# Kernel optimization log

Measured on AMD Instinct MI355X. Metric: run time of the kernel, lower is better.

The kernel has to match this reference:

```python
import jax, jax.numpy as jnp
import numpy as np

# ---- static config (mirrors Spectral2xDown.__init__) ----
B, C_IN, C_OUT = 2, 256, 256
H_HI, W_HI = 256, 512
H_LO, W_LO = 128, 256
LMAX = H_LO            # 128
MMAX = W_LO // 2 + 1   # 129
GROUPS = 32
EPS_GN = 1e-5


def _cc_nodes_weights(n):
    """Clenshaw-Curtis nodes x_j=cos(pi*j/(n-1)) and quadrature weights on [-1,1]
    (torch_harmonics 'equiangular' grid)."""
    N = n - 1
    tj = np.pi * np.arange(n) / N
    xj = np.cos(tj)
    ks = np.arange(1, N // 2 + 1)
    b = np.where(2 * ks == N, 1.0, 2.0)
    s = (b / (4.0 * ks**2 - 1.0))[None, :] * np.cos(2.0 * ks[None, :] * tj[:, None])
    w = (2.0 / N) * (1.0 - s.sum(axis=1))
    w[0] = w[-1] = (1.0 / N**2) if (N % 2) else (1.0 / (N**2 - 1.0))
    return xj, w


def _legpoly(mmax, lmax, x):
    """Orthonormal associated Legendre (-1)^m c_lm P_lm(x), shape [mmax,lmax,len(x)]
    (torch_harmonics _precompute_legpoly, norm='ortho', csphase=True)."""
    nmax = max(mmax, lmax)
    vdm = np.zeros((nmax, nmax, len(x)))
    vdm[0, 0] = 1.0 / np.sqrt(4.0 * np.pi)
    for l in range(1, nmax):
        vdm[l - 1, l] = np.sqrt(2 * l + 1) * x * vdm[l - 1, l - 1]
        vdm[l, l] = np.sqrt((2 * l + 1) * (1 + x) * (1 - x) / (2 * l)) * vdm[l - 1, l - 1]
    for l in range(2, nmax):
        for m in range(0, l - 1):
            vdm[m, l] = (x * np.sqrt((2 * l - 1) / (l - m) * (2 * l + 1) / (l + m)) * vdm[m, l - 1]
                         - np.sqrt((l + m - 1) / (l - m) * (2 * l + 1) / (2 * l - 3)
                                   * (l - m - 1) / (l + m)) * vdm[m, l - 2])
    vdm = vdm[:mmax, :lmax].copy()
    for m in range(1, mmax, 2):  # Condon-Shortley phase
        vdm[m] *= -1.0
    return vdm


def _precompute():
    ct_hi, w_hi = _cc_nodes_weights(H_HI)
    pct_hi = _legpoly(MMAX, LMAX, np.flip(np.arccos(ct_hi)) * 0 + np.cos(np.flip(np.arccos(ct_hi))))
    wmat_hi = pct_hi * w_hi[None, None, :]          # quadrature folded in: [M,L,K_hi]
    ct_lo, _ = _cc_nodes_weights(H_LO)
    pct_lo = _legpoly(MMAX, LMAX, np.cos(np.flip(np.arccos(ct_lo))))  # [M,L,K_lo]
    return wmat_hi.astype(np.float32), pct_lo.astype(np.float32)


def setup_inputs() -> dict:
    key = jax.random.key(0)
    k1, k2 = jax.random.split(key, 2)
    x = jax.random.normal(k1, (B, C_IN, H_HI, W_HI), jnp.float32)
    conv_w = jax.random.normal(k2, (C_OUT, C_IN), jnp.float32) / np.sqrt(C_IN)
    conv_b = jnp.zeros((C_OUT,), jnp.float32)
    gamma = jnp.ones((C_OUT,), jnp.float32)
    beta = jnp.zeros((C_OUT,), jnp.float32)
    wmat_hi, pct_lo = _precompute()
    return {"x": x, "conv_w": conv_w, "conv_b": conv_b, "gamma": gamma, "beta": beta,
            "wmat_hi": jnp.asarray(wmat_hi), "pct_lo": jnp.asarray(pct_lo)}


def reference(x, conv_w, conv_b, gamma, beta, wmat_hi, pct_lo):
    # --- forward real SHT on high-res grid (2*pi * rfft(norm='forward') + Legendre quadrature) ---
    X = (2.0 * jnp.pi / W_HI) * jnp.fft.rfft(x, axis=-1)     # [B,C,K_hi,W_HI//2+1]
    X = X[..., :MMAX]                                        # truncate to mmax
    flm_r = jnp.einsum('bckm,mlk->bclm', X.real, wmat_hi)    # [B,C,L,M]
    flm_i = jnp.einsum('bckm,mlk->bclm', X.imag, wmat_hi)
    # --- inverse real SHT on low-res grid ---
    g = (jnp.einsum('bclm,mlk->bckm', flm_r, pct_lo)
         + 1j * jnp.einsum('bclm,mlk->bckm', flm_i, pct_lo))  # [B,C,K_lo,M]
    y = jnp.fft.irfft(g, n=W_LO, axis=-1) * W_LO             # irfft norm='forward'
    # --- 1x1 conv -> GroupNorm(32) -> exact GELU ---
    h = jnp.einsum('bchw,oc->bohw', y, conv_w) + conv_b[None, :, None, None]
    hg = h.reshape(B, GROUPS, C_OUT // GROUPS, H_LO, W_LO)
    mu = hg.mean(axis=(2, 3, 4), keepdims=True)
    var = ((hg - mu) ** 2).mean(axis=(2, 3, 4), keepdims=True)
    hn = ((hg - mu) * jax.lax.rsqrt(var + EPS_GN)).reshape(B, C_OUT, H_LO, W_LO)
    out = hn * gamma[None, :, None, None] + beta[None, :, None, None]
    return jax.nn.gelu(out, approximate=False)
```

## Files before the change

kernel.cpp:

```cpp
#include <hip/hip_runtime.h>
#include <math.h>


#define ROWS_HI 131072
#define ROWS_LO 65536

#define B_FT    0LL
#define B_FIT   262144LL
#define B_WM    393216LL
#define B_PCT   8781824LL
#define B_STATS 12976128LL
#define B_R1    12976640LL
#define B_R2    80085504LL

typedef __attribute__((ext_vector_type(8))) short bf16x8;
typedef __attribute__((ext_vector_type(8))) unsigned short ushort8;
typedef __attribute__((ext_vector_type(4))) unsigned short ushort4v;
typedef __attribute__((ext_vector_type(4))) float f32x4;

__device__ inline unsigned short f2bf(float f){
  unsigned int u = __float_as_uint(f);
  unsigned int r = u + 0x7FFFu + ((u >> 16) & 1u);
  return (unsigned short)(r >> 16);
}
__device__ inline float bf2f(unsigned short h){
  return __uint_as_float(((unsigned int)h) << 16);
}

__global__ __launch_bounds__(256) void k_tables(unsigned char* __restrict__ ws){
  unsigned short* FT  = (unsigned short*)(ws + B_FT);
  unsigned short* FIT = (unsigned short*)(ws + B_FIT);
  float* stats = (float*)(ws + B_STATS);
  int idx = blockIdx.x*256 + threadIdx.x;
  if (idx < 131072){
    int p = idx >> 9, w = idx & 511, m = p >> 1;
    int pr = (m*w) & 511;
    float ang = (float)pr * (float)(2.0*M_PI/512.0);
    float s, c; sincosf(ang, &s, &c);
    const float S = (float)(2.0*M_PI/512.0);
    FT[idx] = f2bf((p & 1) ? (-S*s) : (S*c));
  }
  int i2 = idx - 131072;
  if (i2 >= 0 && i2 < 65536){
    int w = i2 >> 8, p = i2 & 255, m = p >> 1;
    float eps = (m == 0) ? 1.f : 2.f;
    int pr = (m*w) & 255;
    float ang = (float)pr * (float)(2.0*M_PI/256.0);
    float s, c; sincosf(ang, &s, &c);
    FIT[i2] = f2bf((p & 1) ? (-eps*s) : (eps*c));
  }
  int i3 = idx - (131072 + 65536);
  if (i3 >= 0 && i3 < 128) stats[i3] = 0.f;
}

__global__ __launch_bounds__(256) void k_prep(const float* __restrict__ wmat,
                                              const float* __restrict__ pct,
                                              unsigned char* __restrict__ ws){
  unsigned short* WM = (unsigned short*)(ws + B_WM);
  unsigned short* PT = (unsigned short*)(ws + B_PCT);
  int idx = blockIdx.x*256 + threadIdx.x;
  if (idx < 4194304){
    WM[idx] = f2bf(wmat[idx]);
  } else {
    int j = idx - 4194304;
    if (j < 2097152){
      int m = j >> 14, kp = (j >> 7) & 127, l = j & 127;
      PT[j] = f2bf(pct[m*16384 + l*128 + kp]);
    }
  }
}

template<int AMODE, int CMODE, bool BIAS>
__global__ __launch_bounds__(256) void k_gemm(
    const float* __restrict__ Af,
    const unsigned short* __restrict__ Abf,
    const unsigned short* __restrict__ Bt,
    float* __restrict__ Cf,
    unsigned short* __restrict__ Cbf,
    const float* __restrict__ bias,
    int ldA, int ldB, int ldC, int ksteps,
    long long sA, long long sB, int bzsh, long long sC)
{
  __shared__ unsigned short Ah[128][40];
  __shared__ unsigned short Al[128][40];
  __shared__ unsigned short Bs[128][40];
  const int tid = threadIdx.x;
  const int z = blockIdx.z;
  const long long offA = (long long)z * sA;
  const long long offB = (long long)(z >> bzsh) * sB;
  const long long offC = (long long)z * sC;
  const int row0 = blockIdx.x * 128;
  const int n0   = blockIdx.y * 128;
  const int lane = tid & 63;
  const int wv = tid >> 6;
  const int wm = wv >> 1, wn = wv & 1;
  const int fr = lane & 15, q = lane >> 4;
  const int ms = tid >> 1, half = tid & 1;

  f32x4 acc[4][4];
#pragma unroll
  for (int i=0;i<4;++i)
#pragma unroll
    for (int j=0;j<4;++j) acc[i][j] = (f32x4){0.f,0.f,0.f,0.f};

  for (int ks = 0; ks < ksteps; ++ks){
    const int k0 = ks * 32;
    if (AMODE == 0){
      const float* s = Af + offA + (long long)(row0 + ms) * ldA + k0 + half*16;
      float vv[16];
      *(float4*)(vv+0)  = *(const float4*)(s+0);
      *(float4*)(vv+4)  = *(const float4*)(s+4);
      *(float4*)(vv+8)  = *(const float4*)(s+8);
      *(float4*)(vv+12) = *(const float4*)(s+12);
      ushort8 H0, H1, L0, L1;
#pragma unroll
      for (int j=0;j<8;++j){
        unsigned short h = f2bf(vv[j]);
        H0[j] = h; L0[j] = f2bf(vv[j] - bf2f(h));
        unsigned short h2 = f2bf(vv[8+j]);
        H1[j] = h2; L1[j] = f2bf(vv[8+j] - bf2f(h2));
      }
      *(ushort8*)&Ah[ms][half*16]   = H0;
      *(ushort8*)&Ah[ms][half*16+8] = H1;
      *(ushort8*)&Al[ms][half*16]   = L0;
      *(ushort8*)&Al[ms][half*16+8] = L1;
    } else {
      const unsigned short* s = Abf + offA + (long long)(row0 + ms) * ldA + k0 + half*16;
      *(ushort8*)&Ah[ms][half*16]   = *(const ushort8*)(s);
      *(ushort8*)&Ah[ms][half*16+8] = *(const ushort8*)(s+8);
    }
    {
      const unsigned short* s = Bt + offB + (long long)(n0 + ms) * ldB + k0 + half*16;
      *(ushort8*)&Bs[ms][half*16]   = *(const ushort8*)(s);
      *(ushort8*)&Bs[ms][half*16+8] = *(const ushort8*)(s+8);
    }
    __syncthreads();
    bf16x8 ah[4], al[4];
#pragma unroll
    for (int mt=0;mt<4;++mt){
      ah[mt] = *(const bf16x8*)&Ah[wm*64+mt*16+fr][q*8];
      if (AMODE == 0) al[mt] = *(const bf16x8*)&Al[wm*64+mt*16+fr][q*8];
    }
#pragma unroll
    for (int nt=0;nt<4;++nt){
      bf16x8 bb = *(const bf16x8*)&Bs[wn*64+nt*16+fr][q*8];
#pragma unroll
      for (int mt=0;mt<4;++mt){
        if (AMODE == 0)
          acc[mt][nt] = __builtin_amdgcn_mfma_f32_16x16x32_bf16(al[mt], bb, acc[mt][nt], 0,0,0);
        acc[mt][nt] = __builtin_amdgcn_mfma_f32_16x16x32_bf16(ah[mt], bb, acc[mt][nt], 0,0,0);
      }
    }
    __syncthreads();
  }

  if (CMODE == 0){
#pragma unroll
    for (int mt=0;mt<4;++mt){
      int row = row0 + wm*64 + mt*16 + q*4;
      float bv0=0.f,bv1=0.f,bv2=0.f,bv3=0.f;
      if (BIAS){ bv0=bias[row]; bv1=bias[row+1]; bv2=bias[row+2]; bv3=bias[row+3]; }
#pragma unroll
      for (int nt=0;nt<4;++nt){
        int col = n0 + wn*64 + nt*16 + fr;
        float* dst = Cf + offC + (long long)row * ldC + col;
        dst[0]                 = acc[mt][nt][0] + bv0;
        dst[(long long)ldC]    = acc[mt][nt][1] + bv1;
        dst[(long long)ldC*2]  = acc[mt][nt][2] + bv2;
        dst[(long long)ldC*3]  = acc[mt][nt][3] + bv3;
      }
    }
  } else {
#pragma unroll
    for (int nt=0;nt<4;++nt){
      int colp = n0 + wn*64 + nt*16 + fr;
#pragma unroll
      for (int mt=0;mt<4;++mt){
        int rowb = row0 + wm*64 + mt*16 + q*4;
        ushort4v h;
        h[0] = f2bf(acc[mt][nt][0]);
        h[1] = f2bf(acc[mt][nt][1]);
        h[2] = f2bf(acc[mt][nt][2]);
        h[3] = f2bf(acc[mt][nt][3]);
        *(ushort4v*)&Cbf[(long long)colp * ldC + rowb] = h;
      }
    }
  }
}

__global__ __launch_bounds__(256) void k_tr(const float* __restrict__ g,
                                            float* __restrict__ gT){
  __shared__ float t[64][65];
  const int r0 = blockIdx.x * 64;
  const int p0 = blockIdx.y * 64;
  const int tr = threadIdx.x & 15, tc = threadIdx.x >> 4;
#pragma unroll
  for (int i=0;i<4;++i){
    int pl = tc + i*16;
    float4 v = *(const float4*)(g + (long long)(p0+pl)*ROWS_LO + r0 + tr*4);
    t[pl][tr*4+0]=v.x; t[pl][tr*4+1]=v.y; t[pl][tr*4+2]=v.z; t[pl][tr*4+3]=v.w;
  }
  __syncthreads();
#pragma unroll
  for (int i=0;i<4;++i){
    int rl = tc + i*16;
    float4 w;
    w.x = t[tr*4+0][rl]; w.y = t[tr*4+1][rl]; w.z = t[tr*4+2][rl]; w.w = t[tr*4+3][rl];
    *(float4*)(gT + (long long)(r0+rl)*256 + p0 + tr*4) = w;
  }
}

__global__ __launch_bounds__(256) void k_tr2(const float* __restrict__ y,
                                             unsigned short* __restrict__ yT){
  __shared__ float t[64][65];
  const int s0 = blockIdx.x * 64;
  const int c0 = blockIdx.y * 64;
  const int b  = blockIdx.z;
  const int tr = threadIdx.x & 15, tc = threadIdx.x >> 4;
#pragma unroll
  for (int i=0;i<4;++i){
    int cl = tc + i*16;
    float4 v = *(const float4*)(y + (long long)b*8388608 + (long long)(c0+cl)*32768 + s0 + tr*4);
    t[cl][tr*4+0]=v.x; t[cl][tr*4+1]=v.y; t[cl][tr*4+2]=v.z; t[cl][tr*4+3]=v.w;
  }
  __syncthreads();
#pragma unroll
  for (int i=0;i<4;++i){
    int sl = tc + i*16;
    ushort4v w;
    w[0]=f2bf(t[tr*4+0][sl]); w[1]=f2bf(t[tr*4+1][sl]);
    w[2]=f2bf(t[tr*4+2][sl]); w[3]=f2bf(t[tr*4+3][sl]);
    *(ushort4v*)(yT + (long long)b*8388608 + (long long)(s0+sl)*256 + c0 + tr*4) = w;
  }
}

__global__ __launch_bounds__(256) void k_stats(const float* __restrict__ h,
                                               float* __restrict__ stats){
  const int bg = blockIdx.y;
  const int j  = blockIdx.x;
  const int t  = threadIdx.x;
  const float* base = h + (long long)bg*262144 + j*8192;
  float s = 0.f, ss = 0.f;
#pragma unroll
  for (int i=0;i<8;++i){
    float4 v = *(const float4*)(base + i*1024 + t*4);
    s  += v.x + v.y + v.z + v.w;
    ss += v.x*v.x + v.y*v.y + v.z*v.z + v.w*v.w;
  }
#pragma unroll
  for (int off=32; off>0; off>>=1){
    s  += __shfl_down(s, off, 64);
    ss += __shfl_down(ss, off, 64);
  }
  __shared__ float red[8];
  int wid = t >> 6;
  if ((t & 63) == 0){ red[wid*2] = s; red[wid*2+1] = ss; }
  __syncthreads();
  if (t == 0){
    float S  = red[0]+red[2]+red[4]+red[6];
    float SS = red[1]+red[3]+red[5]+red[7];
    atomicAdd(&stats[bg*2+0], S);
    atomicAdd(&stats[bg*2+1], SS);
  }
}

__global__ __launch_bounds__(256) void k_norm(float* __restrict__ out,
                                              const float* __restrict__ stats,
                                              const float* __restrict__ gamma,
                                              const float* __restrict__ beta){
  long long idx4 = ((long long)blockIdx.x*256 + threadIdx.x)*4;
  int o = (int)((idx4 >> 15) & 255);
  int b = (int)(idx4 >> 23);
  int bg = b*32 + (o >> 3);
  const float inv_n = 1.0f/262144.0f;
  float mean = stats[bg*2+0] * inv_n;
  float var  = stats[bg*2+1] * inv_n - mean*mean;
  float sc = rsqrtf(var + 1e-5f);
  float ga = gamma[o], be = beta[o];
  float4 v = *(float4*)(out + idx4);
  float t0 = (v.x - mean)*sc*ga + be;
  float t1 = (v.y - mean)*sc*ga + be;
  float t2 = (v.z - mean)*sc*ga + be;
  float t3 = (v.w - mean)*sc*ga + be;
  const float ISQ2 = 0.70710678118654752f;
  v.x = 0.5f*t0*(1.0f + erff(t0*ISQ2));
  v.y = 0.5f*t1*(1.0f + erff(t1*ISQ2));
  v.z = 0.5f*t2*(1.0f + erff(t2*ISQ2));
  v.w = 0.5f*t3*(1.0f + erff(t3*ISQ2));
  *(float4*)(out + idx4) = v;
}

extern "C" void kernel_launch(void* const* d_in, const int* in_sizes, int n_in,
                              void* d_out, int out_size, void* d_ws, size_t ws_size,
                              hipStream_t stream){
  const float* x      = (const float*)d_in[0];
  const float* conv_w = (const float*)d_in[1];
  const float* conv_b = (const float*)d_in[2];
  const float* gamma  = (const float*)d_in[3];
  const float* beta   = (const float*)d_in[4];
  const float* wmat   = (const float*)d_in[5];
  const float* pct    = (const float*)d_in[6];
  unsigned char* ws = (unsigned char*)d_ws;

  unsigned short* FT   = (unsigned short*)(ws + B_FT);
  unsigned short* FIT  = (unsigned short*)(ws + B_FIT);
  unsigned short* WM   = (unsigned short*)(ws + B_WM);
  unsigned short* PT   = (unsigned short*)(ws + B_PCT);
  float*          stats= (float*)(ws + B_STATS);
  unsigned short* Xbf  = (unsigned short*)(ws + B_R1);
  float*          g    = (float*)(ws + B_R1);
  float*          y    = (float*)(ws + B_R1);
  float*          flm  = (float*)(ws + B_R2);
  float*          gT   = (float*)(ws + B_R2);
  unsigned short* yT   = (unsigned short*)(ws + B_R2);
  float* out = (float*)d_out;

  k_tables<<<769, 256, 0, stream>>>(ws);
  k_prep  <<<24576, 256, 0, stream>>>(wmat, pct, ws);

  k_gemm<0,1,false><<<dim3(1024,2,1), 256, 0, stream>>>(
      x, nullptr, FT, nullptr, Xbf, nullptr, 512, 512, ROWS_HI, 16, 0, 0, 0, 0);
  k_gemm<1,0,false><<<dim3(4,1,256), 256, 0, stream>>>(
      nullptr, Xbf, WM, flm, nullptr, nullptr, 256, 256, 128, 8,
      (long long)ROWS_HI, 32768LL, 1, (long long)ROWS_LO);
  k_gemm<0,0,false><<<dim3(4,1,256), 256, 0, stream>>>(
      flm, nullptr, PT, g, nullptr, nullptr, 128, 128, 128, 4,
      (long long)ROWS_LO, 16384LL, 1, (long long)ROWS_LO);
  k_tr<<<dim3(1024,4), 256, 0, stream>>>(g, gT);
  k_gemm<0,0,false><<<dim3(512,2,1), 256, 0, stream>>>(
      gT, nullptr, FIT, y, nullptr, nullptr, 256, 256, 256, 8, 0, 0, 0, 0);
  k_tr2<<<dim3(512,4,2), 256, 0, stream>>>(y, yT);
  k_gemm<0,0,true><<<dim3(2,256,2), 256, 0, stream>>>(
      conv_w, nullptr, yT, out, nullptr, conv_b, 256, 256, 32768, 8,
      0, 8388608LL, 0, 8388608LL);

  k_stats<<<dim3(32,64), 256, 0, stream>>>(out, stats);
  k_norm <<<16384, 256, 0, stream>>>(out, stats, gamma, beta);
}
```

Baseline: 699.1 us.

## Drop split-bf16 precision, store intermediates in bf16, skip triangular Legendre work, retile GEMMs

Removes the hi/lo bf16 split of fp32 A operands, so every GEMM issues half as many MFMAs and skips the residual conversion. The flm and g intermediates are now stored as bf16 instead of fp32, and the transpose works on bf16. The Legendre GEMMs skip tiles that are zero by triangularity (l<m), and tile shapes become templated (wider N or M tiles). Conv weights are pre-converted to bf16. Accuracy drops to plain bf16 throughout, which risks exceeding the tolerance.

```diff
diff --git a/kernel.cpp b/kernel.cpp
--- a/kernel.cpp
+++ b/kernel.cpp
@@ -9,9 +9,10 @@
 #define B_FIT   262144LL
 #define B_WM    393216LL
 #define B_PCT   8781824LL
-#define B_STATS 12976128LL
-#define B_R1    12976640LL
-#define B_R2    80085504LL
+#define B_WB    12976128LL
+#define B_STATS 13107200LL
+#define B_R1    13107712LL
+#define B_R2    80216576LL
 
 typedef __attribute__((ext_vector_type(8))) short bf16x8;
 typedef __attribute__((ext_vector_type(8))) unsigned short ushort8;
@@ -22,9 +23,6 @@
   unsigned int u = __float_as_uint(f);
   unsigned int r = u + 0x7FFFu + ((u >> 16) & 1u);
   return (unsigned short)(r >> 16);
-}
-__device__ inline float bf2f(unsigned short h){
-  return __uint_as_float(((unsigned int)h) << 16);
 }
 
 __global__ __launch_bounds__(256) void k_tables(unsigned char* __restrict__ ws){
@@ -55,22 +53,25 @@
 
 __global__ __launch_bounds__(256) void k_prep(const float* __restrict__ wmat,
                                               const float* __restrict__ pct,
+                                              const float* __restrict__ Wc,
                                               unsigned char* __restrict__ ws){
   unsigned short* WM = (unsigned short*)(ws + B_WM);
   unsigned short* PT = (unsigned short*)(ws + B_PCT);
+  unsigned short* WB = (unsigned short*)(ws + B_WB);
   int idx = blockIdx.x*256 + threadIdx.x;
   if (idx < 4194304){
     WM[idx] = f2bf(wmat[idx]);
-  } else {
+  } else if (idx < 6291456){
     int j = idx - 4194304;
-    if (j < 2097152){
-      int m = j >> 14, kp = (j >> 7) & 127, l = j & 127;
-      PT[j] = f2bf(pct[m*16384 + l*128 + kp]);
-    }
-  }
-}
-
-template<int AMODE, int CMODE, bool BIAS>
+    int m = j >> 14, kp = (j >> 7) & 127, l = j & 127;
+    PT[j] = f2bf(pct[m*16384 + l*128 + kp]);
+  } else if (idx < 6356992){
+    int j = idx - 6291456;
+    WB[j] = f2bf(Wc[j]);
+  }
+}
+
+template<int AMODE, int CMODE, bool BIAS, int MT, int NT, int SKIP>
 __global__ __launch_bounds__(256) void k_gemm(
     const float* __restrict__ Af,
     const unsigned short* __restrict__ Abf,
@@ -81,132 +82,152 @@
     int ldA, int ldB, int ldC, int ksteps,
     long long sA, long long sB, int bzsh, long long sC)
 {
-  __shared__ unsigned short Ah[128][40];
-  __shared__ unsigned short Al[128][40];
-  __shared__ unsigned short Bs[128][40];
+  constexpr int BM = MT*32;
+  constexpr int BN = NT*32;
+  __shared__ unsigned short As[BM][40];
+  __shared__ unsigned short Bs[BN][40];
   const int tid = threadIdx.x;
   const int z = blockIdx.z;
+  const int m = z >> 1;
   const long long offA = (long long)z * sA;
   const long long offB = (long long)(z >> bzsh) * sB;
   const long long offC = (long long)z * sC;
-  const int row0 = blockIdx.x * 128;
-  const int n0   = blockIdx.y * 128;
+  const int row0 = blockIdx.x * BM;
+  const int n0   = blockIdx.y * BN;
   const int lane = tid & 63;
   const int wv = tid >> 6;
   const int wm = wv >> 1, wn = wv & 1;
   const int fr = lane & 15, q = lane >> 4;
-  const int ms = tid >> 1, half = tid & 1;
-
-  f32x4 acc[4][4];
-#pragma unroll
-  for (int i=0;i<4;++i)
-#pragma unroll
-    for (int j=0;j<4;++j) acc[i][j] = (f32x4){0.f,0.f,0.f,0.f};
-
-  for (int ks = 0; ks < ksteps; ++ks){
+
+  f32x4 acc[MT][NT];
+#pragma unroll
+  for (int i=0;i<MT;++i)
+#pragma unroll
+    for (int j=0;j<NT;++j) acc[i][j] = (f32x4){0.f,0.f,0.f,0.f};
+
+  int ks0 = (SKIP == 2) ? (m >> 5) : 0;
+  for (int ks = ks0; ks < ksteps; ++ks){
     const int k0 = ks * 32;
     if (AMODE == 0){
-      const float* s = Af + offA + (long long)(row0 + ms) * ldA + k0 + half*16;
+      const int row = tid >> 1, half = tid & 1;
+      const float* s = Af + offA + (long long)(row0 + row) * ldA + k0 + half*16;
       float vv[16];
       *(float4*)(vv+0)  = *(const float4*)(s+0);
       *(float4*)(vv+4)  = *(const float4*)(s+4);
       *(float4*)(vv+8)  = *(const float4*)(s+8);
       *(float4*)(vv+12) = *(const float4*)(s+12);
-      ushort8 H0, H1, L0, L1;
-#pragma unroll
-      for (int j=0;j<8;++j){
-        unsigned short h = f2bf(vv[j]);
-        H0[j] = h; L0[j] = f2bf(vv[j] - bf2f(h));
-        unsigned short h2 = f2bf(vv[8+j]);
-        H1[j] = h2; L1[j] = f2bf(vv[8+j] - bf2f(h2));
-      }
-      *(ushort8*)&Ah[ms][half*16]   = H0;
-      *(ushort8*)&Ah[ms][half*16+8] = H1;
-      *(ushort8*)&Al[ms][half*16]   = L0;
-      *(ushort8*)&Al[ms][half*16+8] = L1;
+      ushort8 H0, H1;
+#pragma unroll
+      for (int j=0;j<8;++j){ H0[j] = f2bf(vv[j]); H1[j] = f2bf(vv[8+j]); }
+      *(ushort8*)&As[row][half*16]   = H0;
+      *(ushort8*)&As[row][half*16+8] = H1;
+    } else if (BM == 256){
+      const unsigned short* s = Abf + offA + (long long)(row0 + tid) * ldA + k0;
+      *(ushort8*)&As[tid][0]  = *(const ushort8*)(s);
+      *(ushort8*)&As[tid][8]  = *(const ushort8*)(s+8);
+      *(ushort8*)&As[tid][16] = *(const ushort8*)(s+16);
+      *(ushort8*)&As[tid][24] = *(const ushort8*)(s+24);
     } else {
-      const unsigned short* s = Abf + offA + (long long)(row0 + ms) * ldA + k0 + half*16;
-      *(ushort8*)&Ah[ms][half*16]   = *(const ushort8*)(s);
-      *(ushort8*)&Ah[ms][half*16+8] = *(const ushort8*)(s+8);
-    }
-    {
-      const unsigned short* s = Bt + offB + (long long)(n0 + ms) * ldB + k0 + half*16;
-      *(ushort8*)&Bs[ms][half*16]   = *(const ushort8*)(s);
-      *(ushort8*)&Bs[ms][half*16+8] = *(const ushort8*)(s+8);
+      const int row = tid >> 1, half = tid & 1;
+      const unsigned short* s = Abf + offA + (long long)(row0 + row) * ldA + k0 + half*16;
+      *(ushort8*)&As[row][half*16]   = *(const ushort8*)(s);
+      *(ushort8*)&As[row][half*16+8] = *(const ushort8*)(s+8);
+    }
+    if (BN == 256){
+      const unsigned short* s = Bt + offB + (long long)(n0 + tid) * ldB + k0;
+      *(ushort8*)&Bs[tid][0]  = *(const ushort8*)(s);
+      *(ushort8*)&Bs[tid][8]  = *(const ushort8*)(s+8);
+      *(ushort8*)&Bs[tid][16] = *(const ushort8*)(s+16);
+      *(ushort8*)&Bs[tid][24] = *(const ushort8*)(s+24);
+    } else {
+      const int row = tid >> 1, half = tid & 1;
+      const unsigned short* s = Bt + offB + (long long)(n0 + row) * ldB + k0 + half*16;
+      *(ushort8*)&Bs[row][half*16]   = *(const ushort8*)(s);
+      *(ushort8*)&Bs[row][half*16+8] = *(const ushort8*)(s+8);
     }
     __syncthreads();
-    bf16x8 ah[4], al[4];
-#pragma unroll
-    for (int mt=0;mt<4;++mt){
-      ah[mt] = *(const bf16x8*)&Ah[wm*64+mt*16+fr][q*8];
-      if (AMODE == 0) al[mt] = *(const bf16x8*)&Al[wm*64+mt*16+fr][q*8];
-    }
-#pragma unroll
-    for (int nt=0;nt<4;++nt){
-      bf16x8 bb = *(const bf16x8*)&Bs[wn*64+nt*16+fr][q*8];
-#pragma unroll
-      for (int mt=0;mt<4;++mt){
-        if (AMODE == 0)
-          acc[mt][nt] = __builtin_amdgcn_mfma_f32_16x16x32_bf16(al[mt], bb, acc[mt][nt], 0,0,0);
+    bf16x8 ah[MT];
+#pragma unroll
+    for (int mt=0;mt<MT;++mt)
+      ah[mt] = *(const bf16x8*)&As[wm*(MT*16)+mt*16+fr][q*8];
+#pragma unroll
+    for (int nt=0;nt<NT;++nt){
+      if (SKIP == 1 && (wn*(NT*16) + nt*16 + 16 <= m)) continue;
+      bf16x8 bb = *(const bf16x8*)&Bs[wn*(NT*16)+nt*16+fr][q*8];
+#pragma unroll
+      for (int mt=0;mt<MT;++mt)
         acc[mt][nt] = __builtin_amdgcn_mfma_f32_16x16x32_bf16(ah[mt], bb, acc[mt][nt], 0,0,0);
-      }
     }
     __syncthreads();
   }
 
   if (CMODE == 0){
 #pragma unroll
-    for (int mt=0;mt<4;++mt){
-      int row = row0 + wm*64 + mt*16 + q*4;
+    for (int mt=0;mt<MT;++mt){
+      int row = row0 + wm*(MT*16) + mt*16 + q*4;
       float bv0=0.f,bv1=0.f,bv2=0.f,bv3=0.f;
       if (BIAS){ bv0=bias[row]; bv1=bias[row+1]; bv2=bias[row+2]; bv3=bias[row+3]; }
 #pragma unroll
-      for (int nt=0;nt<4;++nt){
-        int col = n0 + wn*64 + nt*16 + fr;
+      for (int nt=0;nt<NT;++nt){
+        int col = n0 + wn*(NT*16) + nt*16 + fr;
         float* dst = Cf + offC + (long long)row * ldC + col;
-        dst[0]                 = acc[mt][nt][0] + bv0;
-        dst[(long long)ldC]    = acc[mt][nt][1] + bv1;
-        dst[(long long)ldC*2]  = acc[mt][nt][2] + bv2;
-        dst[(long long)ldC*3]  = acc[mt][nt][3] + bv3;
+        dst[0]                = acc[mt][nt][0] + bv0;
+        dst[(long long)ldC]   = acc[mt][nt][1] + bv1;
+        dst[(long long)ldC*2] = acc[mt][nt][2] + bv2;
+        dst[(long long)ldC*3] = acc[mt][nt][3] + bv3;
       }
     }
-  } else {
-#pragma unroll
-    for (int nt=0;nt<4;++nt){
-      int colp = n0 + wn*64 + nt*16 + fr;
-#pragma unroll
-      for (int mt=0;mt<4;++mt){
-        int rowb = row0 + wm*64 + mt*16 + q*4;
+  } else if (CMODE == 1){
+#pragma unroll
+    for (int nt=0;nt<NT;++nt){
+      int colp = n0 + wn*(NT*16) + nt*16 + fr;
+#pragma unroll
+      for (int mt=0;mt<MT;++mt){
+        int rowb = row0 + wm*(MT*16) + mt*16 + q*4;
         ushort4v h;
         h[0] = f2bf(acc[mt][nt][0]);
         h[1] = f2bf(acc[mt][nt][1]);
         h[2] = f2bf(acc[mt][nt][2]);
         h[3] = f2bf(acc[mt][nt][3]);
-        *(ushort4v*)&Cbf[(long long)colp * ldC + rowb] = h;
+        *(ushort4v*)&Cbf[offC + (long long)colp * ldC + rowb] = h;
       }
     }
-  }
-}
-
-__global__ __launch_bounds__(256) void k_tr(const float* __restrict__ g,
-                                            float* __restrict__ gT){
-  __shared__ float t[64][65];
+  } else {
+#pragma unroll
+    for (int mt=0;mt<MT;++mt){
+      int row = row0 + wm*(MT*16) + mt*16 + q*4;
+#pragma unroll
+      for (int nt=0;nt<NT;++nt){
+        int col = n0 + wn*(NT*16) + nt*16 + fr;
+        unsigned short* dst = Cbf + offC + (long long)row * ldC + col;
+        dst[0]      = f2bf(acc[mt][nt][0]);
+        dst[ldC]    = f2bf(acc[mt][nt][1]);
+        dst[ldC*2]  = f2bf(acc[mt][nt][2]);
+        dst[ldC*3]  = f2bf(acc[mt][nt][3]);
+      }
+    }
+  }
+}
+
+__global__ __launch_bounds__(256) void k_trb(const unsigned short* __restrict__ g,
+                                             unsigned short* __restrict__ gT){
+  __shared__ unsigned short t[64][68];
   const int r0 = blockIdx.x * 64;
   const int p0 = blockIdx.y * 64;
   const int tr = threadIdx.x & 15, tc = threadIdx.x >> 4;
 #pragma unroll
   for (int i=0;i<4;++i){
     int pl = tc + i*16;
-    float4 v = *(const float4*)(g + (long long)(p0+pl)*ROWS_LO + r0 + tr*4);
-    t[pl][tr*4+0]=v.x; t[pl][tr*4+1]=v.y; t[pl][tr*4+2]=v.z; t[pl][tr*4+3]=v.w;
+    ushort4v v = *(const ushort4v*)(g + (long long)(p0+pl)*ROWS_LO + r0 + tr*4);
+    *(ushort4v*)&t[pl][tr*4] = v;
   }
   __syncthreads();
 #pragma unroll
   for (int i=0;i<4;++i){
     int rl = tc + i*16;
-    float4 w;
-    w.x = t[tr*4+0][rl]; w.y = t[tr*4+1][rl]; w.z = t[tr*4+2][rl]; w.w = t[tr*4+3][rl];
-    *(float4*)(gT + (long long)(r0+rl)*256 + p0 + tr*4) = w;
+    ushort4v w;
+    w[0]=t[tr*4+0][rl]; w[1]=t[tr*4+1][rl]; w[2]=t[tr*4+2][rl]; w[3]=t[tr*4+3][rl];
+    *(ushort4v*)(gT + (long long)(r0+rl)*256 + p0 + tr*4) = w;
   }
 }
 
@@ -306,32 +327,33 @@
   unsigned short* FIT  = (unsigned short*)(ws + B_FIT);
   unsigned short* WM   = (unsigned short*)(ws + B_WM);
   unsigned short* PT   = (unsigned short*)(ws + B_PCT);
+  unsigned short* WB   = (unsigned short*)(ws + B_WB);
   float*          stats= (float*)(ws + B_STATS);
   unsigned short* Xbf  = (unsigned short*)(ws + B_R1);
-  float*          g    = (float*)(ws + B_R1);
+  unsigned short* gb   = (unsigned short*)(ws + B_R1);
   float*          y    = (float*)(ws + B_R1);
-  float*          flm  = (float*)(ws + B_R2);
-  float*          gT   = (float*)(ws + B_R2);
+  unsigned short* flmb = (unsigned short*)(ws + B_R2);
+  unsigned short* gTb  = (unsigned short*)(ws + B_R2);
   unsigned short* yT   = (unsigned short*)(ws + B_R2);
   float* out = (float*)d_out;
 
   k_tables<<<769, 256, 0, stream>>>(ws);
-  k_prep  <<<24576, 256, 0, stream>>>(wmat, pct, ws);
-
-  k_gemm<0,1,false><<<dim3(1024,2,1), 256, 0, stream>>>(
+  k_prep  <<<24832, 256, 0, stream>>>(wmat, pct, conv_w, ws);
+
+  k_gemm<0,1,false,4,8,0><<<dim3(1024,1,1), 256, 0, stream>>>(
       x, nullptr, FT, nullptr, Xbf, nullptr, 512, 512, ROWS_HI, 16, 0, 0, 0, 0);
-  k_gemm<1,0,false><<<dim3(4,1,256), 256, 0, stream>>>(
-      nullptr, Xbf, WM, flm, nullptr, nullptr, 256, 256, 128, 8,
-      (long long)ROWS_HI, 32768LL, 1, (long long)ROWS_LO);
-  k_gemm<0,0,false><<<dim3(4,1,256), 256, 0, stream>>>(
-      flm, nullptr, PT, g, nullptr, nullptr, 128, 128, 128, 4,
-      (long long)ROWS_LO, 16384LL, 1, (long long)ROWS_LO);
-  k_tr<<<dim3(1024,4), 256, 0, stream>>>(g, gT);
-  k_gemm<0,0,false><<<dim3(512,2,1), 256, 0, stream>>>(
-      gT, nullptr, FIT, y, nullptr, nullptr, 256, 256, 256, 8, 0, 0, 0, 0);
+  k_gemm<1,2,false,4,4,1><<<dim3(4,1,256), 256, 0, stream>>>(
+      nullptr, Xbf, WM, nullptr, flmb, nullptr, 256, 256, 128, 8,
+      131072LL, 32768LL, 1, 65536LL);
+  k_gemm<1,2,false,4,4,2><<<dim3(4,1,256), 256, 0, stream>>>(
+      nullptr, flmb, PT, nullptr, gb, nullptr, 128, 128, 128, 4,
+      65536LL, 16384LL, 1, 65536LL);
+  k_trb<<<dim3(1024,4), 256, 0, stream>>>(gb, gTb);
+  k_gemm<1,0,false,4,8,0><<<dim3(512,1,1), 256, 0, stream>>>(
+      nullptr, gTb, FIT, y, nullptr, nullptr, 256, 256, 256, 8, 0, 0, 0, 0);
   k_tr2<<<dim3(512,4,2), 256, 0, stream>>>(y, yT);
-  k_gemm<0,0,true><<<dim3(2,256,2), 256, 0, stream>>>(
-      conv_w, nullptr, yT, out, nullptr, conv_b, 256, 256, 32768, 8,
+  k_gemm<1,0,true,8,4,0><<<dim3(1,256,2), 256, 0, stream>>>(
+      nullptr, WB, yT, out, nullptr, conv_b, 256, 256, 32768, 8,
       0, 8388608LL, 0, 8388608LL);
 
   k_stats<<<dim3(32,64), 256, 0, stream>>>(out, stats);
```

Measured after the change: 670.5 us. 1.04x faster.
